# Kernel tuning notes

Measured on AMD Instinct MI355X. Metric: run time of the kernel, lower is better.

The kernel has to match this reference:

```python
import jax, jax.numpy as jnp
import numpy as np

N_NODES = 100000
N_USER = 50000
D_IN = 100     # n_units[0]
F_OUT = 16     # n_units[1]
N_HEAD = 3     # n_heads[0]
N_TYPES = 3    # nb_nodes
N_EDGES = 1600000
D2 = 128


def setup_inputs() -> dict:
    key = jax.random.key(0)
    ks = jax.random.split(key, 9)
    h = jax.random.normal(ks[0], (N_NODES, D_IN), dtype=jnp.float32)
    edge_index = jax.random.randint(ks[1], (N_TYPES, 2, N_EDGES), 0, N_NODES, dtype=jnp.int64)
    # per-type GAT params (torch Linear stored transposed: (in, out))
    W = jax.random.normal(ks[2], (N_TYPES, D_IN, N_HEAD * F_OUT), dtype=jnp.float32) * 0.1
    b = jax.random.normal(ks[3], (N_TYPES, N_HEAD * F_OUT), dtype=jnp.float32) * 0.1
    a_src = jax.random.normal(ks[4], (N_TYPES, N_HEAD, F_OUT), dtype=jnp.float32) * 0.1
    a_trg = jax.random.normal(ks[5], (N_TYPES, N_HEAD, F_OUT), dtype=jnp.float32) * 0.1
    # additive attention params
    w1 = jax.random.normal(ks[6], (D_IN, D2), dtype=jnp.float32) * 0.1
    w2 = jax.random.normal(ks[7], (F_OUT, D2), dtype=jnp.float32) * 0.1
    m = jax.random.normal(ks[8], (D2, 1), dtype=jnp.float32) * 0.1
    return {"h": h, "W": W, "b": b, "a_src": a_src, "a_trg": a_trg,
            "w1": w1, "w2": w2, "m": m, "edge_index": edge_index}


def _sparse_gat(h, src, trg, W, b, a_src, a_trg):
    """Single SparseMultiHeadGraphAttention layer followed by head-mean."""
    N = h.shape[0]
    h_prime = (h @ W + b).reshape(N, N_HEAD, F_OUT)  # (N, H, F)
    hs = h_prime[src]                                # (E', H, F) edge gather
    # NOTE: faithful to source — both scores use the src-gathered features
    e = (hs * a_src).sum(-1) + (hs * a_trg).sum(-1)  # (E', H)
    e = jax.nn.leaky_relu(e, negative_slope=0.2)
    e = e - e.max()                                  # global max (as in source)
    exp_e = jnp.exp(e)
    denom = jax.ops.segment_sum(exp_e, trg, num_segments=N)      # (N, H)
    alpha = exp_e / (denom[trg] + 1e-10)                          # (E', H)
    out = jax.ops.segment_sum(hs * alpha[..., None], trg, num_segments=N)  # (N, H, F)
    return out.mean(axis=1)  # == permute(1,0,2).mean(dim=0)


def reference(h, W, b, a_src, a_trg, w1, w2, m, edge_index):
    N = h.shape[0]
    loop = jnp.arange(N, dtype=edge_index.dtype)
    embs = []
    for t in range(N_TYPES):  # small fixed set of relation types
        src = jnp.concatenate([edge_index[t, 0], loop])  # add self-loops
        trg = jnp.concatenate([edge_index[t, 1], loop])
        x = _sparse_gat(h, src, trg, W[t], b[t], a_src[t], a_trg[t])
        embs.append(x[:N_USER])
    type_aware = jnp.stack(embs, axis=1)  # (Nu, |Rs|, F)
    feat = h[:N_USER]                     # (Nu, D)
    # additive attention over types
    q = jnp.tanh((feat @ w1)[:, None, :] + type_aware @ w2)  # (Nu, |Rs|, D2)
    scores = (q @ m)[..., 0]                                  # (Nu, |Rs|)
    beta = jax.nn.softmax(scores, axis=1)
    fusion = jnp.einsum('nr,nrf->nf', beta, type_aware)[:, None, :]  # (Nu,1,F)
    return jnp.concatenate([fusion, type_aware], axis=1)  # (Nu, |Rs|+1, F)
```

## Files before the change

kernel.cpp:

```cpp
#include <hip/hip_runtime.h>
#include <hip/hip_bf16.h>

#define N_NODES 100000
#define N_USER  50000
#define D_IN    100
#define F_OUT   16
#define N_HEAD  3
#define N_TYPES 3
#define N_EDGES 1600000
#define D2      128
#define N_SEG   (N_TYPES * N_USER)
#define KP      136
#define CAP     64
#define CAPH    32
#define NBLK    ((N_NODES + 63) / 64)
#define NPAIR   (N_TYPES * N_EDGES / 2)
#define NBIN    256
#define SEGB    586
#define NBLKA   782
#define PAIRS_A 3072
#define CAPPB   40
#define NPREPB  270
#define NPLACE  512

typedef __hip_bfloat16 bf16;
typedef __attribute__((ext_vector_type(8))) short bf16x8;
typedef __attribute__((ext_vector_type(4))) float f32x4;
static __device__ __forceinline__ float b2f(bf16 x) { return __bfloat162float(x); }

#define OFF_CVT   64
#define OFF_CW    (OFF_CVT)
#define OFF_CB    (OFF_CW + 14400)
#define OFF_CAS   (OFF_CB + 144)
#define OFF_CAT   (OFF_CAS + 144)
#define OFF_CW1   (OFF_CAT + 144)
#define OFF_CW2   (OFF_CW1 + 12800)
#define OFF_CM    (OFF_CW2 + 2048)
#define CVT_TOTAL 29808
#define OFF_WT    29888
#define OFF_REC   49472
#define OFF_BUCKET (OFF_REC + 9600000 + 240000 + 302000 + 9600000 + 2400000 + 6406144)
#define OFF_CPB   (OFF_REC + 9600000)
#define OFF_CA    (OFF_CPB + 240000)
#define OFF_CB2   (OFF_CA + 151000)
#define OFF_ELIST (OFF_CB2 + 151000)
#define OFF_TA    (OFF_ELIST + 9600000)
#define OFF_FW1   (OFF_TA + 2400000)

__global__ void k_detect(const unsigned* __restrict__ hraw,
                         const unsigned* __restrict__ eiraw,
                         int* __restrict__ flags) {
    __shared__ int sane, nz;
    if (threadIdx.x == 0) { sane = 0; nz = 0; }
    __syncthreads();
    int cnt = 0; unsigned o = 0;
    for (int i = threadIdx.x; i < 1024; i += 256) {
        unsigned w = hraw[i];
        unsigned e = (w >> 23) & 0xFF;
        if (e >= 64 && e <= 200) cnt++;
        o |= eiraw[2 * i + 1];
    }
    atomicAdd(&sane, cnt);
    atomicOr(&nz, (int)(o != 0));
    __syncthreads();
    if (threadIdx.x == 0) {
        flags[0] = (sane > 512) ? 1 : 0;
        flags[1] = nz ? 0 : 1;
    }
}

static __device__ __forceinline__ int2 load_ei2(const void* ei, int f64, size_t pairPos) {
    if (f64) {
        int4 v = ((const int4*)ei)[pairPos];
        int2 r; r.x = v.x; r.y = v.z; return r;
    }
    return ((const int2*)ei)[pairPos];
}

#define NBLK_CVT 117
__global__ __launch_bounds__(256) void k_prep_part(
        const void* __restrict__ W, const void* __restrict__ b,
        const void* __restrict__ as_, const void* __restrict__ at_,
        const void* __restrict__ w1, const void* __restrict__ w2,
        const void* __restrict__ m, const void* __restrict__ ei,
        const int* __restrict__ flags,
        float* __restrict__ cvt, ushort* __restrict__ wt,
        unsigned* __restrict__ bucket, unsigned* __restrict__ cpb) {
    __shared__ int bc[NBIN];
    const int tid = threadIdx.x;
    if (blockIdx.x < NBLK_CVT) {
        int i = blockIdx.x * 256 + tid;
        if (i >= CVT_TOTAL) return;
        const void* src; int off;
        if      (i < 14400)                 { src = W;   off = i; }
        else if (i < 14400+144)             { src = b;   off = i - 14400; }
        else if (i < 14400+288)             { src = as_; off = i - 14544; }
        else if (i < 14400+432)             { src = at_; off = i - 14688; }
        else if (i < 14400+432+12800)       { src = w1;  off = i - 14832; }
        else if (i < 14400+432+12800+2048)  { src = w2;  off = i - 27632; }
        else                                { src = m;   off = i - 29680; }
        cvt[i] = flags[0] ? ((const float*)src)[off] : b2f(((const bf16*)src)[off]);
    } else if (blockIdx.x < NPREPB) {
        int i = (blockIdx.x - NBLK_CVT) * 256 + tid;
        if (i >= 6 * 48 * KP) return;
        int g = i / (48 * KP);
        int r = i - g * (48 * KP);
        int n = r / KP, k = r % KP;
        ushort v = 0;
        if (k < D_IN) {
            if (g < 3) {
                size_t src = ((size_t)g * D_IN + k) * 48 + n;
                if (flags[0]) { bf16 x = __float2bfloat16(((const float*)W)[src]); v = *(ushort*)&x; }
                else          { v = ((const ushort*)W)[src]; }
            } else {
                int c = (g - 3) * 48 + n;
                if (c < D2) {
                    size_t src = (size_t)k * D2 + c;
                    if (flags[0]) { bf16 x = __float2bfloat16(((const float*)w1)[src]); v = *(ushort*)&x; }
                    else          { v = ((const ushort*)w1)[src]; }
                }
            }
        }
        wt[i] = v;
    } else {
        const int blk = blockIdx.x - NPREPB;
        const int f64ei = flags[1];
        const int NE2 = N_EDGES >> 1;
        if (tid < NBIN) bc[tid] = 0;
        __syncthreads();
        const int pair0 = blk * PAIRS_A;
        int npair = NPAIR - pair0; if (npair > PAIRS_A) npair = PAIRS_A;
#pragma unroll
        for (int q = 0; q < PAIRS_A / 256; ++q) {
            int pp = q * 256 + tid;
            int ok = (pp < npair);
            int pg = pair0 + (ok ? pp : 0);
            int t  = (pg >= 2 * NE2) ? 2 : ((pg >= NE2) ? 1 : 0);
            int ep = pg - t * NE2;
            int2 tg = load_ei2(ei, f64ei, (size_t)(t * 2 + 1) * NE2 + ep);
            int2 sr = load_ei2(ei, f64ei, (size_t)(t * 2) * NE2 + ep);
            if (ok && (unsigned)tg.x < N_USER) {
                int seg = t * N_USER + tg.x;
                int bin = seg & 255;
                int pos = atomicAdd(&bc[bin], 1);
                if (pos < CAPPB)
                    bucket[((size_t)bin * NBLKA + blk) * CAPPB + pos] =
                        ((unsigned)(seg >> 8) << 17) | (unsigned)sr.x;
            }
            if (ok && (unsigned)tg.y < N_USER) {
                int seg = t * N_USER + tg.y;
                int bin = seg & 255;
                int pos = atomicAdd(&bc[bin], 1);
                if (pos < CAPPB)
                    bucket[((size_t)bin * NBLKA + blk) * CAPPB + pos] =
                        ((unsigned)(seg >> 8) << 17) | (unsigned)sr.y;
            }
        }
        __syncthreads();
        if (tid < NBIN) cpb[(size_t)tid * NBLKA + blk] = (unsigned)bc[tid];
    }
}

__global__ __launch_bounds__(256) void k_place_pack(
        const unsigned* __restrict__ bucket, const unsigned* __restrict__ cpb,
        int* __restrict__ elist, unsigned* __restrict__ cA,
        unsigned* __restrict__ cBv,
        const void* __restrict__ h, const ushort* __restrict__ wtg,
        const float* __restrict__ cb, const float* __restrict__ cas,
        const float* __restrict__ cat, const int* __restrict__ flags,
        float* __restrict__ fw1G, float* __restrict__ rec) {
    __shared__ alignas(16) unsigned char smem[26624];
    const int tid = threadIdx.x;
    if (blockIdx.x < NPLACE) {
        int* sc = (int*)smem;
        const int bin = blockIdx.x >> 1;
        const int hf  = blockIdx.x & 1;
        for (int i = tid; i < SEGB; i += 256) sc[i] = 0;
        __syncthreads();
        const int rn = NBLKA / 2;
        for (int j = tid; j < rn; j += 256) {
            int r = 2 * j + hf;
            int c = (int)cpb[(size_t)bin * NBLKA + r];
            if (c > CAPPB) c = CAPPB;
            size_t base = ((size_t)bin * NBLKA + r) * CAPPB;
            for (int i4 = 0; i4 < (c + 3) >> 2; ++i4) {
                uint4 wv = *(const uint4*)&bucket[base + 4 * i4];
#pragma unroll
                for (int k = 0; k < 4; ++k) {
                    int idx = 4 * i4 + k;
                    if (idx < c) {
                        unsigned e = (k == 0) ? wv.x : (k == 1) ? wv.y : (k == 2) ? wv.z : wv.w;
                        int sl  = (int)(e >> 17);
                        int src = (int)(e & 0x1FFFFu);
                        int pos = atomicAdd(&sc[sl], 1);
                        if (pos < CAPH) {
                            int seg = (sl << 8) + bin;
                            int t = seg / N_USER;
                            elist[(size_t)seg * CAP + (hf << 5) + pos] =
                                (t * N_NODES + src) << 7;
                        }
                    }
                }
            }
        }
        __syncthreads();
        for (int s = tid; s < SEGB; s += 256) {
            int seg = (s << 8) + bin;
            if (seg < N_SEG) {
                int cc = sc[s]; if (cc > CAPH) cc = CAPH;
                if (hf) cBv[seg] = (unsigned)cc; else cA[seg] = (unsigned)cc;
            }
        }
    } else {
        ushort (*hs)[KP] = reinterpret_cast<ushort(*)[KP]>(smem);
        unsigned* img = (unsigned*)(smem + 17408);
        const int node0 = (blockIdx.x - NPLACE) * 64;
        const int f32in = flags[0];
        if (f32in) {
            const float* hfp = (const float*)h;
            for (int i = tid; i < 64 * 25; i += 256) {
                int r = i / 25, ch = i - r * 25;
                int n = node0 + r;
                ushort4 s4 = make_ushort4(0, 0, 0, 0);
                if (n < N_NODES) {
                    float4 x = *(const float4*)&hfp[(size_t)n * D_IN + ch * 4];
                    bf16 b0 = __float2bfloat16(x.x), b1 = __float2bfloat16(x.y);
                    bf16 b2 = __float2bfloat16(x.z), b3 = __float2bfloat16(x.w);
                    s4 = make_ushort4(*(ushort*)&b0, *(ushort*)&b1, *(ushort*)&b2, *(ushort*)&b3);
                }
                *(ushort4*)&hs[r][ch * 4] = s4;
            }
        } else {
            const ushort* hu = (const ushort*)h;
            for (int i = tid; i < 64 * 25; i += 256) {
                int r = i / 25, ch = i - r * 25;
                int n = node0 + r;
                uint2 v = make_uint2(0, 0);
                if (n < N_NODES)
                    v = *(const uint2*)&hu[(size_t)n * D_IN + ch * 4];
                *(uint2*)&hs[r][ch * 4] = v;
            }
        }
        for (int i = tid; i < 64 * 9; i += 256) {
            int r = i / 9, ch = i - r * 9;
            *(uint2*)&hs[r][100 + ch * 4] = make_uint2(0, 0);
        }
        __syncthreads();
        const int lane = tid & 63;
        const int w    = tid >> 6;
        const int m    = lane & 15;
        const int quad = lane >> 4;
        ushort* img16 = (ushort*)img;
        const int elig = (node0 < N_USER);
        const int nphase = elig ? 6 : 3;
        for (int p = 0; p < nphase; ++p) {
            const ushort* wp = wtg + (size_t)p * 48 * KP;
            f32x4 acc0 = {0.f, 0.f, 0.f, 0.f}, acc1 = acc0, acc2 = acc0;
#pragma unroll
            for (int ks = 0; ks < 4; ++ks) {
                int ko = ks * 32 + quad * 8;
                bf16x8 a  = *(const bf16x8*)&hs[w * 16 + m][ko];
                bf16x8 b0 = *(const bf16x8*)&wp[(0 * 16 + m) * KP + ko];
                bf16x8 b1 = *(const bf16x8*)&wp[(1 * 16 + m) * KP + ko];
                bf16x8 b2 = *(const bf16x8*)&wp[(2 * 16 + m) * KP + ko];
                acc0 = __builtin_amdgcn_mfma_f32_16x16x32_bf16(a, b0, acc0, 0, 0, 0);
                acc1 = __builtin_amdgcn_mfma_f32_16x16x32_bf16(a, b1, acc1, 0, 0, 0);
                acc2 = __builtin_amdgcn_mfma_f32_16x16x32_bf16(a, b2, acc2, 0, 0, 0);
            }
            if (p < 3) {
                const int t = p;
                float hpv[3][4], sred[3][4];
#pragma unroll
                for (int nt = 0; nt < 3; ++nt) {
                    int col = nt * 16 + m;
                    float bv = cb[t * 48 + col];
                    float av = cas[t * 48 + col] + cat[t * 48 + col];
                    f32x4 a4 = (nt == 0) ? acc0 : (nt == 1) ? acc1 : acc2;
#pragma unroll
                    for (int r = 0; r < 4; ++r) {
                        hpv[nt][r] = a4[r] + bv;
                        sred[nt][r] = hpv[nt][r] * av;
                    }
                }
#pragma unroll
                for (int d = 1; d < 16; d <<= 1) {
#pragma unroll
                    for (int nt = 0; nt < 3; ++nt)
#pragma unroll
                        for (int r = 0; r < 4; ++r)
                            sred[nt][r] += __shfl_xor(sred[nt][r], d);
                }
                float pk[3][4];
#pragma unroll
                for (int nt = 0; nt < 3; ++nt)
#pragma unroll
                    for (int r = 0; r < 4; ++r) {
                        float s = sred[nt][r];
                        s = (s > 0.f) ? s : 0.2f * s;
                        pk[nt][r] = __expf(s);
                    }
                __syncthreads();
#pragma unroll
                for (int nt = 0; nt < 3; ++nt) {
                    int col = nt * 16 + m;
#pragma unroll
                    for (int r = 0; r < 4; ++r) {
                        int row = w * 16 + quad * 4 + r;
                        bf16 gb = __float2bfloat16(pk[nt][r] * hpv[nt][r]);
                        img16[row * 72 + col] = *(ushort*)&gb;
                    }
                }
                if (m < 8) {
#pragma unroll
                    for (int r = 0; r < 4; ++r) {
                        int row = w * 16 + quad * 4 + r;
                        img[row * 36 + 24 + m] = (m < 3) ? __float_as_uint(pk[m][r]) : 0u;
                    }
                }
                __syncthreads();
                {
                    int r = tid >> 2, q = tid & 3;
                    int n = node0 + r;
                    if (n < N_NODES) {
                        const uint4* s = (const uint4*)&img[r * 36 + q * 8];
                        uint4 x0 = s[0], x1 = s[1];
                        uint4* d = (uint4*)((unsigned*)rec + ((size_t)t * N_NODES + n) * 32 + q * 8);
                        d[0] = x0; d[1] = x1;
                    }
                }
            } else {
                const int chunk = p - 3;
#pragma unroll
                for (int nt = 0; nt < 3; ++nt) {
                    int col = chunk * 48 + nt * 16 + m;
                    if (col < D2) {
                        f32x4 a4 = (nt == 0) ? acc0 : (nt == 1) ? acc1 : acc2;
#pragma unroll
                        for (int r = 0; r < 4; ++r) {
                            int row = w * 16 + quad * 4 + r;
                            int v = node0 + row;
                            if (v < N_USER) fw1G[(size_t)v * D2 + col] = a4[r];
                        }
                    }
                }
            }
        }
    }
}

__global__ __launch_bounds__(256) void k_gather(const float* __restrict__ rec,
                                                const int* __restrict__ elist,
                                                const unsigned* __restrict__ cA,
                                                const unsigned* __restrict__ cBv,
                                                float* __restrict__ ta) {
    int wid = (blockIdx.x * 256 + threadIdx.x) >> 6;
    if (wid >= N_SEG) return;
    int lane = threadIdx.x & 63;
    int t = wid / N_USER, v = wid - t * N_USER;
    int h = lane >> 5, l = lane & 31;
    const char* recc = (const char*)rec;
    const unsigned l4 = (unsigned)(l << 2);
    const bool isg = (l < 24);
    const int      s0m = isg ? 16 : 0;
    const unsigned m0  = isg ? 0xFFFF0000u : 0xFFFFFFFFu;
    const unsigned m1  = isg ? 0xFFFF0000u : 0u;
    int ev = elist[(size_t)wid * CAP + lane];
    int a = (int)cA[wid];
    int b = (int)cBv[wid];
    unsigned wself = 0u;
    if (h == 0)
        wself = *(const unsigned*)(recc + (((unsigned)(t * N_NODES + v)) << 7) + l4);
    float a0 = 0.f, a1 = 0.f;
    const int myn = h ? b : a;
    const int mx = a > b ? a : b;
    const int hbase = h << 5;
    for (int i0 = 0; i0 < mx; i0 += 12) {
        unsigned w[12];
#pragma unroll
        for (int q = 0; q < 12; ++q) {
            w[q] = 0u;
            int ee = i0 + q;
            int off = __shfl(ev, hbase + (ee & 31));
            if (ee < myn)
                w[q] = *(const unsigned*)(recc + (unsigned)off + l4);
        }
        __builtin_amdgcn_sched_barrier(0);
#pragma unroll
        for (int q = 0; q < 12; ++q) {
            a0 += __uint_as_float((w[q] << s0m) & m0);
            a1 += __uint_as_float(w[q] & m1);
        }
    }
    a0 += __uint_as_float((wself << s0m) & m0);
    a1 += __uint_as_float(wself & m1);
    a0 += __shfl_xor(a0, 32);
    a1 += __shfl_xor(a1, 32);
    int k = (l >> 3); if (k > 2) k = 2;
    float dk = __shfl(a0, 24 + k) + 1e-10f;
    float r0 = a0 / dk, r1 = a1 / dk;
    float sf0 = r0 + __shfl(r0, (l & 7) + 8) + __shfl(r0, (l & 7) + 16);
    float sf1 = r1 + __shfl(r1, (l & 7) + 8) + __shfl(r1, (l & 7) + 16);
    if (lane < 8) {
        float2 o;
        o.x = sf0 * (1.f / 3.f);
        o.y = sf1 * (1.f / 3.f);
        *(float2*)&ta[(size_t)v * 48 + t * 16 + 2 * lane] = o;
    }
}

__global__ __launch_bounds__(256) void k_fuse(const float* __restrict__ fw1G,
                                              const float* __restrict__ cw2,
                                              const float* __restrict__ cm,
                                              const float* __restrict__ ta,
                                              const int* __restrict__ flags,
                                              void* __restrict__ out) {
    __shared__ float w2s[F_OUT * D2];
    __shared__ float ms[D2];
    __shared__ float tas[64][49];
    __shared__ float psum[64][12];
    __shared__ float fus[64][16];
    const int tid = threadIdx.x;
    const int v0 = blockIdx.x * 64;
    const int f32in = flags[0];
    for (int i = tid; i < F_OUT * D2; i += 256) w2s[i] = cw2[i];
    if (tid < D2) ms[tid] = cm[tid];
    {
        int r = tid >> 2, c4 = (tid & 3) * 12;
        int v = v0 + r;
        for (int j = 0; j < 12; ++j)
            tas[r][c4 + j] = (v < N_USER) ? ta[(size_t)v * 48 + c4 + j] : 0.f;
    }
    __syncthreads();
    const int u  = tid & 63;
    const int og = tid >> 6;
    const int v  = v0 + u;
    float tr[48];
#pragma unroll
    for (int x = 0; x < 48; ++x) tr[x] = tas[u][x];
    float acc[2][16];
#pragma unroll
    for (int ph = 0; ph < 2; ++ph) {
        if (v < N_USER) {
            const float4* fr = (const float4*)&fw1G[(size_t)v * D2 + ph * 64 + og * 16];
#pragma unroll
            for (int q = 0; q < 4; ++q) {
                float4 x = fr[q];
                acc[ph][q * 4 + 0] = x.x;
                acc[ph][q * 4 + 1] = x.y;
                acc[ph][q * 4 + 2] = x.z;
                acc[ph][q * 4 + 3] = x.w;
            }
        } else {
#pragma unroll
            for (int j = 0; j < 16; ++j) acc[ph][j] = 0.f;
        }
    }
    float part[3] = {0.f, 0.f, 0.f};
#pragma unroll
    for (int ph = 0; ph < 2; ++ph) {
#pragma unroll
        for (int j = 0; j < 16; ++j) {
            int c = ph * 64 + og * 16 + j;
            float fv = acc[ph][j];
            float mv = ms[c];
#pragma unroll
            for (int t = 0; t < 3; ++t) {
                float z = fv;
#pragma unroll
                for (int f = 0; f < 16; ++f)
                    z += tr[t * 16 + f] * w2s[f * D2 + c];
                float q = 1.f - 2.f / (__expf(2.f * z) + 1.f);
                part[t] += q * mv;
            }
        }
    }
    psum[u][og * 3 + 0] = part[0];
    psum[u][og * 3 + 1] = part[1];
    psum[u][og * 3 + 2] = part[2];
    __syncthreads();
    if (tid < 64) {
        float sc[3];
#pragma unroll
        for (int t = 0; t < 3; ++t)
            sc[t] = psum[tid][t] + psum[tid][3 + t] + psum[tid][6 + t] + psum[tid][9 + t];
        float mx = fmaxf(sc[0], fmaxf(sc[1], sc[2]));
        float e0 = __expf(sc[0] - mx), e1 = __expf(sc[1] - mx), e2 = __expf(sc[2] - mx);
        float inv = 1.f / (e0 + e1 + e2);
#pragma unroll
        for (int f = 0; f < 16; ++f)
            fus[tid][f] = (e0 * tas[tid][f] + e1 * tas[tid][16 + f] + e2 * tas[tid][32 + f]) * inv;
    }
    __syncthreads();
    for (int kq = 0; kq < 16; ++kq) {
        int lin = kq * 256 + tid;
        int r = lin >> 6, c = lin & 63;
        int vv = v0 + r;
        if (vv < N_USER) {
            float val = (c < 16) ? fus[r][c] : tas[r][c - 16];
            size_t oidx = (size_t)vv * 64 + c;
            if (f32in) ((float*)out)[oidx] = val;
            else       ((bf16*)out)[oidx]  = __float2bfloat16(val);
        }
    }
}

extern "C" void kernel_launch(void* const* d_in, const int* in_sizes, int n_in,
                              void* d_out, int out_size, void* d_ws, size_t ws_size,
                              hipStream_t stream) {
    float* ws = (float*)d_ws;
    int*   flags = (int*)ws;
    float* cvt   = ws + OFF_CVT;
    float* cb    = ws + OFF_CB;
    float* cas   = ws + OFF_CAS;
    float* cat   = ws + OFF_CAT;
    float* cw2   = ws + OFF_CW2;
    float* cm    = ws + OFF_CM;
    ushort* wt   = (ushort*)(ws + OFF_WT);
    float* rec   = ws + OFF_REC;
    unsigned* bucket = (unsigned*)(ws + OFF_BUCKET);
    unsigned* cpb    = (unsigned*)(ws + OFF_CPB);
    unsigned* cA     = (unsigned*)(ws + OFF_CA);
    unsigned* cBv    = (unsigned*)(ws + OFF_CB2);
    int*   elist = (int*)(ws + OFF_ELIST);
    float* ta    = ws + OFF_TA;
    float* fw1   = ws + OFF_FW1;

    k_detect<<<1, 256, 0, stream>>>((const unsigned*)d_in[0], (const unsigned*)d_in[8], flags);

    k_prep_part<<<NPREPB + NBLKA, 256, 0, stream>>>(
        d_in[1], d_in[2], d_in[3], d_in[4], d_in[5], d_in[6], d_in[7], d_in[8],
        flags, cvt, wt, bucket, cpb);

    k_place_pack<<<NPLACE + NBLK, 256, 0, stream>>>(
        bucket, cpb, elist, cA, cBv,
        d_in[0], wt, cb, cas, cat, flags, fw1, rec);

    k_gather<<<(N_SEG * 64 + 255) / 256, 256, 0, stream>>>(rec, elist, cA, cBv, ta);

    k_fuse<<<(N_USER + 63) / 64, 256, 0, stream>>>(fw1, cw2, cm, ta, flags, d_out);
}
```

Baseline: 347.9 us.

## Write GAT records directly to global and store fw1 projection in bf16

The pack phase no longer stages each node's bf16 features and exp-scores in a shared-memory image before copying them out with vectorized stores. Each lane now writes its bf16 elements and score floats straight to the global record buffer, which removes two block barriers and shrinks shared memory. The feat@w1 intermediate is now stored as bf16 instead of fp32 and expanded in k_fuse, halving that traffic. The cost is many scattered 2-byte global stores in place of coalesced 16-byte ones, plus reduced precision in the tanh input.

```diff
diff --git a/kernel.cpp b/kernel.cpp
--- a/kernel.cpp
+++ b/kernel.cpp
@@ -27,6 +27,7 @@
 typedef __attribute__((ext_vector_type(8))) short bf16x8;
 typedef __attribute__((ext_vector_type(4))) float f32x4;
 static __device__ __forceinline__ float b2f(bf16 x) { return __bfloat162float(x); }
+static __device__ __forceinline__ float us2f(ushort u) { return __uint_as_float(((unsigned)u) << 16); }
 
 #define OFF_CVT   64
 #define OFF_CW    (OFF_CVT)
@@ -168,8 +169,8 @@
         const void* __restrict__ h, const ushort* __restrict__ wtg,
         const float* __restrict__ cb, const float* __restrict__ cas,
         const float* __restrict__ cat, const int* __restrict__ flags,
-        float* __restrict__ fw1G, float* __restrict__ rec) {
-    __shared__ alignas(16) unsigned char smem[26624];
+        ushort* __restrict__ fw1G, float* __restrict__ rec) {
+    __shared__ alignas(16) unsigned char smem[17408];
     const int tid = threadIdx.x;
     if (blockIdx.x < NPLACE) {
         int* sc = (int*)smem;
@@ -213,7 +214,6 @@
         }
     } else {
         ushort (*hs)[KP] = reinterpret_cast<ushort(*)[KP]>(smem);
-        unsigned* img = (unsigned*)(smem + 17408);
         const int node0 = (blockIdx.x - NPLACE) * 64;
         const int f32in = flags[0];
         if (f32in) {
@@ -250,9 +250,9 @@
         const int w    = tid >> 6;
         const int m    = lane & 15;
         const int quad = lane >> 4;
-        ushort* img16 = (ushort*)img;
         const int elig = (node0 < N_USER);
         const int nphase = elig ? 6 : 3;
+        char* recc = (char*)rec;
         for (int p = 0; p < nphase; ++p) {
             const ushort* wp = wtg + (size_t)p * 48 * KP;
             f32x4 acc0 = {0.f, 0.f, 0.f, 0.f}, acc1 = acc0, acc2 = acc0;
@@ -299,33 +299,24 @@
                         s = (s > 0.f) ? s : 0.2f * s;
                         pk[nt][r] = __expf(s);
                     }
-                __syncthreads();
 #pragma unroll
                 for (int nt = 0; nt < 3; ++nt) {
-                    int col = nt * 16 + m;
+                    int colb = (nt * 16 + m) * 2;
 #pragma unroll
                     for (int r = 0; r < 4; ++r) {
-                        int row = w * 16 + quad * 4 + r;
-                        bf16 gb = __float2bfloat16(pk[nt][r] * hpv[nt][r]);
-                        img16[row * 72 + col] = *(ushort*)&gb;
+                        int n = node0 + w * 16 + quad * 4 + r;
+                        if (n < N_NODES) {
+                            bf16 gb = __float2bfloat16(pk[nt][r] * hpv[nt][r]);
+                            *(ushort*)(recc + (((size_t)t * N_NODES + n) << 7) + colb) = *(ushort*)&gb;
+                        }
                     }
                 }
-                if (m < 8) {
+                if (m < 3) {
 #pragma unroll
                     for (int r = 0; r < 4; ++r) {
-                        int row = w * 16 + quad * 4 + r;
-                        img[row * 36 + 24 + m] = (m < 3) ? __float_as_uint(pk[m][r]) : 0u;
-                    }
-                }
-                __syncthreads();
-                {
-                    int r = tid >> 2, q = tid & 3;
-                    int n = node0 + r;
-                    if (n < N_NODES) {
-                        const uint4* s = (const uint4*)&img[r * 36 + q * 8];
-                        uint4 x0 = s[0], x1 = s[1];
-                        uint4* d = (uint4*)((unsigned*)rec + ((size_t)t * N_NODES + n) * 32 + q * 8);
-                        d[0] = x0; d[1] = x1;
+                        int n = node0 + w * 16 + quad * 4 + r;
+                        if (n < N_NODES)
+                            *(float*)(recc + (((size_t)t * N_NODES + n) << 7) + 96 + m * 4) = pk[m][r];
                     }
                 }
             } else {
@@ -339,7 +330,10 @@
                         for (int r = 0; r < 4; ++r) {
                             int row = w * 16 + quad * 4 + r;
                             int v = node0 + row;
-                            if (v < N_USER) fw1G[(size_t)v * D2 + col] = a4[r];
+                            if (v < N_USER) {
+                                bf16 fb = __float2bfloat16(a4[r]);
+                                fw1G[(size_t)v * D2 + col] = *(ushort*)&fb;
+                            }
                         }
                     }
                 }
@@ -408,7 +402,7 @@
     }
 }
 
-__global__ __launch_bounds__(256) void k_fuse(const float* __restrict__ fw1G,
+__global__ __launch_bounds__(256) void k_fuse(const ushort* __restrict__ fw1G,
                                               const float* __restrict__ cw2,
                                               const float* __restrict__ cm,
                                               const float* __restrict__ ta,
@@ -441,15 +435,12 @@
 #pragma unroll
     for (int ph = 0; ph < 2; ++ph) {
         if (v < N_USER) {
-            const float4* fr = (const float4*)&fw1G[(size_t)v * D2 + ph * 64 + og * 16];
-#pragma unroll
-            for (int q = 0; q < 4; ++q) {
-                float4 x = fr[q];
-                acc[ph][q * 4 + 0] = x.x;
-                acc[ph][q * 4 + 1] = x.y;
-                acc[ph][q * 4 + 2] = x.z;
-                acc[ph][q * 4 + 3] = x.w;
-            }
+            const ushort* fr = fw1G + (size_t)v * D2 + ph * 64 + og * 16;
+            ushort us[16];
+            *(uint4*)&us[0] = *(const uint4*)&fr[0];
+            *(uint4*)&us[8] = *(const uint4*)&fr[8];
+#pragma unroll
+            for (int j = 0; j < 16; ++j) acc[ph][j] = us2f(us[j]);
         } else {
 #pragma unroll
             for (int j = 0; j < 16; ++j) acc[ph][j] = 0.f;
@@ -523,7 +514,7 @@
     unsigned* cBv    = (unsigned*)(ws + OFF_CB2);
     int*   elist = (int*)(ws + OFF_ELIST);
     float* ta    = ws + OFF_TA;
-    float* fw1   = ws + OFF_FW1;
+    ushort* fw1  = (ushort*)(ws + OFF_FW1);
 
     k_detect<<<1, 256, 0, stream>>>((const unsigned*)d_in[0], (const unsigned*)d_in[8], flags);
 
```

Result: no change. 350.4 us (+0.7%).
